# Optimization experiments

Hardware: AMD Instinct MI355X
Metric: run time of the kernel (lower is better)

## Reference

```python
import jax, jax.numpy as jnp
import numpy as np

N, D, H, M = 8192, 64, 4096, 2
EPS = 1e-12  # F.normalize eps


def setup_inputs() -> dict:
    key = jax.random.key(0)
    k0, k1, k2, k3, k4 = jax.random.split(key, 5)
    # spins in {-1, +1}
    x = (2 * jax.random.randint(k0, (N, D), 0, 2) - 1).astype(jnp.float32)
    W1 = jax.random.normal(k1, (D, H), jnp.float32) * 0.05
    b1 = jax.random.normal(k2, (H,), jnp.float32) * 0.05
    W2 = jax.random.normal(k3, (H, M), jnp.float32) * 0.05
    b2 = jax.random.normal(k4, (M,), jnp.float32) * 0.05
    return {"x": x, "W1": W1, "b1": b1, "W2": W2, "b2": b2}


def reference(x, W1, b1, W2, b2):
    # Per step d: mask off sites >= d, run MLP, L2-normalize the 2 amplitudes,
    # select psi_pos/psi_neg by the spin at site d, accumulate product.
    n, d_sites = x.shape
    site_idx = jnp.arange(d_sites)

    def step(wav, d):
        mask = (site_idx < d).astype(x.dtype)          # [D], sites 0..d-1 visible
        h = jnp.tanh((x * mask) @ W1 + b1)             # [N, H]
        out = jnp.tanh(h @ W2 + b2)                    # [N, 2]
        norm = jnp.maximum(
            jnp.sqrt(jnp.sum(out * out, axis=1, keepdims=True)), EPS)
        out = out / norm                               # F.normalize(out, 2)
        sel = jnp.where(x[:, d] > 0, out[:, 0], out[:, 1])
        return wav * sel, None

    wav0 = jnp.ones((n,), x.dtype)
    wav, _ = jax.lax.scan(step, wav0, jnp.arange(d_sites))
    return wav
```

## Files before the change

### kernel.cpp

```cpp
#include <hip/hip_runtime.h>
#include <math.h>

#define NS 8192
#define DS 64
#define HD 4096
#define C2L 2.8853900817779268f
#define CH 4
#define NCH (DS / CH)

typedef float v2f __attribute__((ext_vector_type(2)));

__device__ __forceinline__ v2f pk_add(v2f a, v2f b) {
    v2f d; asm("v_pk_add_f32 %0, %1, %2" : "=v"(d) : "v"(a), "v"(b)); return d;
}
__device__ __forceinline__ v2f pk_mul(v2f a, v2f b) {
    v2f d; asm("v_pk_mul_f32 %0, %1, %2" : "=v"(d) : "v"(a), "v"(b)); return d;
}
__device__ __forceinline__ v2f pk_fma(v2f a, v2f b, v2f c) {
    v2f d; asm("v_pk_fma_f32 %0, %1, %2, %3" : "=v"(d) : "v"(a), "v"(b), "v"(c)); return d;
}

__device__ __forceinline__ float fast_tanh(float x) {
    float t = __builtin_amdgcn_exp2f(x * C2L);
    float r = __builtin_amdgcn_rcpf(t + 1.0f);
    return __builtin_fmaf(-2.0f, r, 1.0f);
}

template <int PATT>
__device__ __forceinline__ v2f swz_xor(v2f v) {
    v2f d;
    d.x = __int_as_float(__builtin_amdgcn_ds_swizzle(__float_as_int(v.x), PATT));
    d.y = __int_as_float(__builtin_amdgcn_ds_swizzle(__float_as_int(v.y), PATT));
    return d;
}

__global__ __launch_bounds__(256) void qnade_prep_E(
    const float* __restrict__ W1, float* __restrict__ Et)
{
    int i = blockIdx.x * 256 + threadIdx.x;
    float w = W1[i] * C2L;
    Et[i]           = __builtin_amdgcn_exp2f(w);
    Et[DS * HD + i] = __builtin_amdgcn_exp2f(-w);
}

__global__ __launch_bounds__(256) void qnade_prep_S(
    const float* __restrict__ W2, const float* __restrict__ b2, float* __restrict__ C01)
{
    __shared__ float p0[4], p1[4];
    int tid = threadIdx.x;
    float s0 = 0.0f, s1 = 0.0f;
    for (int h = tid; h < HD; h += 256) {
        float2 w = ((const float2*)W2)[h];
        s0 += w.x; s1 += w.y;
    }
    #pragma unroll
    for (int m = 1; m < 64; m <<= 1) {
        s0 += __shfl_xor(s0, m, 64);
        s1 += __shfl_xor(s1, m, 64);
    }
    if ((tid & 63) == 0) { p0[tid >> 6] = s0; p1[tid >> 6] = s1; }
    __syncthreads();
    if (tid == 0) {
        C01[0] = p0[0] + p0[1] + p0[2] + p0[3] + b2[0];
        C01[1] = p1[0] + p1[1] + p1[2] + p1[3] + b2[1];
    }
}

#define EV(S, N) e##S##N
#define TV(S, N) t##S##N

#define CHAIN(S, MIDX, SLOT) do {                                             \
    v2f q1 = pk_add(TV(S,0), one);                                            \
    v2f q2 = pk_fma(q1, TV(S,1), q1);                                         \
    v2f q3 = pk_fma(q2, TV(S,2), q2);                                         \
    v2f q4 = pk_fma(q3, TV(S,3), q3);                                         \
    v2f q5 = pk_fma(q4, TV(S,4), q4);                                         \
    v2f q6 = pk_fma(q5, TV(S,5), q5);                                         \
    v2f q7 = pk_fma(q6, TV(S,6), q6);                                         \
    v2f q8 = pk_fma(q7, TV(S,7), q7);                                         \
    float P = q8.x * q8.y;                                                    \
    float R = __builtin_amdgcn_rcpf(P);                                       \
    v2f RR = (v2f){R * q8.y, R * q8.x};                                       \
    v2f r7 = pk_mul(RR, q7);                                                  \
    v2f A0 = pk_mul(r7, w20[7]);                                              \
    v2f A1 = pk_mul(r7, w21[7]);                                              \
    RR = pk_fma(RR, TV(S,7), RR);                                             \
    v2f r6 = pk_mul(RR, q6); A0 = pk_fma(r6, w20[6], A0); A1 = pk_fma(r6, w21[6], A1); RR = pk_fma(RR, TV(S,6), RR); \
    v2f r5 = pk_mul(RR, q5); A0 = pk_fma(r5, w20[5], A0); A1 = pk_fma(r5, w21[5], A1); RR = pk_fma(RR, TV(S,5), RR); \
    v2f r4 = pk_mul(RR, q4); A0 = pk_fma(r4, w20[4], A0); A1 = pk_fma(r4, w21[4], A1); RR = pk_fma(RR, TV(S,4), RR); \
    v2f r3 = pk_mul(RR, q3); A0 = pk_fma(r3, w20[3], A0); A1 = pk_fma(r3, w21[3], A1); RR = pk_fma(RR, TV(S,3), RR); \
    v2f r2 = pk_mul(RR, q2); A0 = pk_fma(r2, w20[2], A0); A1 = pk_fma(r2, w21[2], A1); RR = pk_fma(RR, TV(S,2), RR); \
    v2f r1 = pk_mul(RR, q1); A0 = pk_fma(r1, w20[1], A0); A1 = pk_fma(r1, w21[1], A1); RR = pk_fma(RR, TV(S,1), RR); \
    A0 = pk_fma(RR, w20[0], A0); A1 = pk_fma(RR, w21[0], A1);                 \
    parts[SLOT][MIDX][tid] = make_float2(A0.x + A0.y, A1.x + A1.y);           \
} while (0)

#define TUPD(S) do {                                                          \
    TV(S,0) = pk_mul(TV(S,0), (v2f){EV(S,0).x, EV(S,0).y});                   \
    TV(S,1) = pk_mul(TV(S,1), (v2f){EV(S,0).z, EV(S,0).w});                   \
    TV(S,2) = pk_mul(TV(S,2), (v2f){EV(S,1).x, EV(S,1).y});                   \
    TV(S,3) = pk_mul(TV(S,3), (v2f){EV(S,1).z, EV(S,1).w});                   \
    TV(S,4) = pk_mul(TV(S,4), (v2f){EV(S,2).x, EV(S,2).y});                   \
    TV(S,5) = pk_mul(TV(S,5), (v2f){EV(S,2).z, EV(S,2).w});                   \
    TV(S,6) = pk_mul(TV(S,6), (v2f){EV(S,3).x, EV(S,3).y});                   \
    TV(S,7) = pk_mul(TV(S,7), (v2f){EV(S,3).z, EV(S,3).w});                   \
} while (0)

#define LOADE(S) do {                                                         \
    unsigned off_ = (((msk##S >> nd) & 1ull) ? 0u : (unsigned)(DS * HD)) + nd * (unsigned)HD; \
    const float4* ep_ = (const float4*)(Et + off_) + tq;                      \
    EV(S,0) = ep_[0]; EV(S,1) = ep_[256]; EV(S,2) = ep_[512]; EV(S,3) = ep_[768]; \
} while (0)

__global__ __launch_bounds__(256, 2) void qnade_main(
    const float* __restrict__ x, const float* __restrict__ b1,
    const float* __restrict__ W2, const float* __restrict__ Et,
    const float* __restrict__ C01, float* __restrict__ out)
{
    __shared__ float2 parts[CH][4][256];
    __shared__ float2 fin[4][DS];

    const int tid  = threadIdx.x;
    const int lane = tid & 63;
    const int wv   = tid >> 6;
    const int n0   = blockIdx.x * 4;
    const int eb   = tid * 4;
    const int tq   = tid;

    v2f w20[8], w21[8];
    #pragma unroll
    for (int q = 0; q < 4; ++q) {
        const float4* p = (const float4*)(W2 + 2 * (eb + q * 1024));
        float4 A = p[0], B = p[1];
        w20[2*q]   = (v2f){A.x, A.z};  w21[2*q]   = (v2f){A.y, A.w};
        w20[2*q+1] = (v2f){B.x, B.z};  w21[2*q+1] = (v2f){B.y, B.w};
    }

    v2f i0, i1, i2, i3, i4, i5, i6, i7;
    {
        float4 ba = *(const float4*)(b1 + eb);
        float4 bb = *(const float4*)(b1 + eb + 1024);
        float4 bc = *(const float4*)(b1 + eb + 2048);
        float4 bd = *(const float4*)(b1 + eb + 3072);
        i0 = (v2f){__builtin_amdgcn_exp2f(ba.x * C2L), __builtin_amdgcn_exp2f(ba.y * C2L)};
        i1 = (v2f){__builtin_amdgcn_exp2f(ba.z * C2L), __builtin_amdgcn_exp2f(ba.w * C2L)};
        i2 = (v2f){__builtin_amdgcn_exp2f(bb.x * C2L), __builtin_amdgcn_exp2f(bb.y * C2L)};
        i3 = (v2f){__builtin_amdgcn_exp2f(bb.z * C2L), __builtin_amdgcn_exp2f(bb.w * C2L)};
        i4 = (v2f){__builtin_amdgcn_exp2f(bc.x * C2L), __builtin_amdgcn_exp2f(bc.y * C2L)};
        i5 = (v2f){__builtin_amdgcn_exp2f(bc.z * C2L), __builtin_amdgcn_exp2f(bc.w * C2L)};
        i6 = (v2f){__builtin_amdgcn_exp2f(bd.x * C2L), __builtin_amdgcn_exp2f(bd.y * C2L)};
        i7 = (v2f){__builtin_amdgcn_exp2f(bd.z * C2L), __builtin_amdgcn_exp2f(bd.w * C2L)};
    }
    v2f tA0=i0,tA1=i1,tA2=i2,tA3=i3,tA4=i4,tA5=i5,tA6=i6,tA7=i7;
    v2f tB0=i0,tB1=i1,tB2=i2,tB3=i3,tB4=i4,tB5=i5,tB6=i6,tB7=i7;
    v2f tC0=i0,tC1=i1,tC2=i2,tC3=i3,tC4=i4,tC5=i5,tC6=i6,tC7=i7;
    v2f tD0=i0,tD1=i1,tD2=i2,tD3=i3,tD4=i4,tD5=i5,tD6=i6,tD7=i7;

    const unsigned long long mskA = __ballot(x[(n0 + 0) * DS + lane] > 0.0f);
    const unsigned long long mskB = __ballot(x[(n0 + 1) * DS + lane] > 0.0f);
    const unsigned long long mskC = __ballot(x[(n0 + 2) * DS + lane] > 0.0f);
    const unsigned long long mskD = __ballot(x[(n0 + 3) * DS + lane] > 0.0f);
    const v2f one = (v2f){1.0f, 1.0f};

    float4 eA0, eA1, eA2, eA3, eB0, eB1, eB2, eB3;
    float4 eC0, eC1, eC2, eC3, eD0, eD1, eD2, eD3;

    unsigned nd = 0;
    LOADE(A); LOADE(B); LOADE(C); LOADE(D);

    int d = 0;
    for (int cc = 0; cc < NCH; ++cc) {
        for (int s4 = 0; s4 < CH; ++s4, ++d) {
            CHAIN(A, 0, s4);
            CHAIN(B, 1, s4);
            CHAIN(C, 2, s4);
            CHAIN(D, 3, s4);
            TUPD(A); TUPD(B); TUPD(C); TUPD(D);
            nd = (unsigned)(d + 1) & (DS - 1);
            LOADE(A); LOADE(B); LOADE(C); LOADE(D);
        }

        __syncthreads();
        {
            const int j  = tid & 15;
            const int u  = tid >> 4;
            const int m  = u & 3;
            const int sr = u >> 2;
            v2f s = (v2f){0.0f, 0.0f};
            #pragma unroll
            for (int i = 0; i < 16; ++i) {
                float2 v = parts[sr][m][j + 16 * i];
                s = pk_add(s, (v2f){v.x, v.y});
            }
            s = pk_add(s, swz_xor<0x041F>(s));
            s = pk_add(s, swz_xor<0x081F>(s));
            s = pk_add(s, swz_xor<0x101F>(s));
            s = pk_add(s, swz_xor<0x201F>(s));
            if (j == 0) fin[m][cc * CH + sr] = make_float2(s.x, s.y);
        }
        __syncthreads();
    }

    {
        const unsigned long long mm = (wv == 0) ? mskA : (wv == 1) ? mskB
                                    : (wv == 2) ? mskC : mskD;
        float2 sv = fin[wv][lane];
        float dot0 = __builtin_fmaf(-2.0f, sv.x, C01[0]);
        float dot1 = __builtin_fmaf(-2.0f, sv.y, C01[1]);
        float o0 = fast_tanh(dot0);
        float o1 = fast_tanh(dot1);
        float nrm = sqrtf(__builtin_fmaf(o0, o0, o1 * o1));
        nrm = fmaxf(nrm, 1e-12f);
        float sel = ((mm >> lane) & 1ull) ? o0 : o1;
        float v = sel * __builtin_amdgcn_rcpf(nrm);
        v *= __shfl_xor(v, 1, 64);
        v *= __shfl_xor(v, 2, 64);
        v *= __shfl_xor(v, 4, 64);
        v *= __shfl_xor(v, 8, 64);
        v *= __shfl_xor(v, 16, 64);
        v *= __shfl_xor(v, 32, 64);
        if (lane == 0) out[n0 + wv] = v;
    }
}

__global__ __launch_bounds__(256) void qnade_fallback(
    const float* __restrict__ x, const float* __restrict__ W1,
    const float* __restrict__ b1, const float* __restrict__ W2,
    const float* __restrict__ b2, float* __restrict__ out)
{
    __shared__ __align__(16) float w20s[HD];
    __shared__ __align__(16) float w21s[HD];
    const int tid = threadIdx.x;
    for (int i = tid; i < HD; i += 256) {
        float2 w = ((const float2*)W2)[i];
        w20s[i] = w.x;
        w21s[i] = w.y;
    }
    const int lane = tid & 63;
    const int wv   = tid >> 6;
    const int n    = (blockIdx.x << 2) + wv;
    const float b20 = b2[0];
    const float b21 = b2[1];
    const float xv = x[n * DS + lane];
    float4 a[16];
    const float4* b1v = (const float4*)b1;
    #pragma unroll
    for (int q = 0; q < 16; ++q) a[q] = b1v[q * 64 + lane];
    __syncthreads();
    const float4* w20v = (const float4*)w20s;
    const float4* w21v = (const float4*)w21s;
    float wav = 1.0f;
    for (int d = 0; d < DS; ++d) {
        const float xd = __shfl(xv, d, 64);
        const float4* w1v = (const float4*)(W1 + d * HD);
        float dot0 = 0.0f, dot1 = 0.0f;
        #pragma unroll
        for (int q = 0; q < 16; ++q) {
            float4 w1 = w1v[q * 64 + lane];
            float4 av = a[q];
            float h0 = fast_tanh(av.x);
            float h1 = fast_tanh(av.y);
            float h2 = fast_tanh(av.z);
            float h3 = fast_tanh(av.w);
            float4 c0 = w20v[q * 64 + lane];
            float4 c1 = w21v[q * 64 + lane];
            dot0 = fmaf(h0, c0.x, dot0); dot0 = fmaf(h1, c0.y, dot0);
            dot0 = fmaf(h2, c0.z, dot0); dot0 = fmaf(h3, c0.w, dot0);
            dot1 = fmaf(h0, c1.x, dot1); dot1 = fmaf(h1, c1.y, dot1);
            dot1 = fmaf(h2, c1.z, dot1); dot1 = fmaf(h3, c1.w, dot1);
            av.x = fmaf(xd, w1.x, av.x); av.y = fmaf(xd, w1.y, av.y);
            av.z = fmaf(xd, w1.z, av.z); av.w = fmaf(xd, w1.w, av.w);
            a[q] = av;
        }
        #pragma unroll
        for (int m = 1; m < 64; m <<= 1) {
            dot0 += __shfl_xor(dot0, m, 64);
            dot1 += __shfl_xor(dot1, m, 64);
        }
        float o0 = fast_tanh(dot0 + b20);
        float o1 = fast_tanh(dot1 + b21);
        float nrm = sqrtf(fmaf(o0, o0, o1 * o1));
        nrm = fmaxf(nrm, 1e-12f);
        float sel = (xd > 0.0f) ? o0 : o1;
        wav *= sel / nrm;
    }
    out[n] = wav;
}

extern "C" void kernel_launch(void* const* d_in, const int* in_sizes, int n_in,
                              void* d_out, int out_size, void* d_ws, size_t ws_size,
                              hipStream_t stream) {
    const float* x  = (const float*)d_in[0];
    const float* W1 = (const float*)d_in[1];
    const float* b1 = (const float*)d_in[2];
    const float* W2 = (const float*)d_in[3];
    const float* b2 = (const float*)d_in[4];
    float* out = (float*)d_out;

    const size_t need = (size_t)(2 * DS * HD + 2) * sizeof(float);
    if (ws_size >= need) {
        float* Et  = (float*)d_ws;
        float* C01 = Et + 2 * DS * HD;
        hipLaunchKernelGGL(qnade_prep_E, dim3(DS * HD / 256), dim3(256), 0, stream, W1, Et);
        hipLaunchKernelGGL(qnade_prep_S, dim3(1), dim3(256), 0, stream, W2, b2, C01);
        hipLaunchKernelGGL(qnade_main, dim3(NS / 4), dim3(256), 0, stream, x, b1, W2, Et, C01, out);
    } else {
        hipLaunchKernelGGL(qnade_fallback, dim3(NS / 4), dim3(256), 0, stream, x, W1, b1, W2, b2, out);
    }
}
```

Measured before the change: 426.3 us.

## Process two samples per block with double-buffered E loads and higher occupancy

```diff
diff --git a/kernel.cpp b/kernel.cpp
--- a/kernel.cpp
+++ b/kernel.cpp
@@ -5,7 +5,7 @@
 #define DS 64
 #define HD 4096
 #define C2L 2.8853900817779268f
-#define CH 4
+#define CH 8
 #define NCH (DS / CH)
 
 typedef float v2f __attribute__((ext_vector_type(2)));
@@ -66,8 +66,9 @@
     }
 }
 
+#define TV(S, N) t##S##N
 #define EV(S, N) e##S##N
-#define TV(S, N) t##S##N
+#define FV(S, N) f##S##N
 
 #define CHAIN(S, MIDX, SLOT) do {                                             \
     v2f q1 = pk_add(TV(S,0), one);                                            \
@@ -92,10 +93,10 @@
     v2f r2 = pk_mul(RR, q2); A0 = pk_fma(r2, w20[2], A0); A1 = pk_fma(r2, w21[2], A1); RR = pk_fma(RR, TV(S,2), RR); \
     v2f r1 = pk_mul(RR, q1); A0 = pk_fma(r1, w20[1], A0); A1 = pk_fma(r1, w21[1], A1); RR = pk_fma(RR, TV(S,1), RR); \
     A0 = pk_fma(RR, w20[0], A0); A1 = pk_fma(RR, w21[0], A1);                 \
-    parts[SLOT][MIDX][tid] = make_float2(A0.x + A0.y, A1.x + A1.y);           \
-} while (0)
-
-#define TUPD(S) do {                                                          \
+    parts[MIDX][SLOT][tid] = make_float2(A0.x + A0.y, A1.x + A1.y);           \
+} while (0)
+
+#define TUPD_E(S) do {                                                        \
     TV(S,0) = pk_mul(TV(S,0), (v2f){EV(S,0).x, EV(S,0).y});                   \
     TV(S,1) = pk_mul(TV(S,1), (v2f){EV(S,0).z, EV(S,0).w});                   \
     TV(S,2) = pk_mul(TV(S,2), (v2f){EV(S,1).x, EV(S,1).y});                   \
@@ -106,90 +107,109 @@
     TV(S,7) = pk_mul(TV(S,7), (v2f){EV(S,3).z, EV(S,3).w});                   \
 } while (0)
 
-#define LOADE(S) do {                                                         \
+#define TUPD_F(S) do {                                                        \
+    TV(S,0) = pk_mul(TV(S,0), (v2f){FV(S,0).x, FV(S,0).y});                   \
+    TV(S,1) = pk_mul(TV(S,1), (v2f){FV(S,0).z, FV(S,0).w});                   \
+    TV(S,2) = pk_mul(TV(S,2), (v2f){FV(S,1).x, FV(S,1).y});                   \
+    TV(S,3) = pk_mul(TV(S,3), (v2f){FV(S,1).z, FV(S,1).w});                   \
+    TV(S,4) = pk_mul(TV(S,4), (v2f){FV(S,2).x, FV(S,2).y});                   \
+    TV(S,5) = pk_mul(TV(S,5), (v2f){FV(S,2).z, FV(S,2).w});                   \
+    TV(S,6) = pk_mul(TV(S,6), (v2f){FV(S,3).x, FV(S,3).y});                   \
+    TV(S,7) = pk_mul(TV(S,7), (v2f){FV(S,3).z, FV(S,3).w});                   \
+} while (0)
+
+#define LOAD_E(S) do {                                                        \
     unsigned off_ = (((msk##S >> nd) & 1ull) ? 0u : (unsigned)(DS * HD)) + nd * (unsigned)HD; \
     const float4* ep_ = (const float4*)(Et + off_) + tq;                      \
-    EV(S,0) = ep_[0]; EV(S,1) = ep_[256]; EV(S,2) = ep_[512]; EV(S,3) = ep_[768]; \
-} while (0)
-
-__global__ __launch_bounds__(256, 2) void qnade_main(
+    EV(S,0) = ep_[0]; EV(S,1) = ep_[64]; EV(S,2) = ep_[128]; EV(S,3) = ep_[192]; \
+} while (0)
+
+#define LOAD_F(S) do {                                                        \
+    unsigned off_ = (((msk##S >> nd) & 1ull) ? 0u : (unsigned)(DS * HD)) + nd * (unsigned)HD; \
+    const float4* ep_ = (const float4*)(Et + off_) + tq;                      \
+    FV(S,0) = ep_[0]; FV(S,1) = ep_[64]; FV(S,2) = ep_[128]; FV(S,3) = ep_[192]; \
+} while (0)
+
+__global__ __launch_bounds__(256, 3) void qnade_main(
     const float* __restrict__ x, const float* __restrict__ b1,
     const float* __restrict__ W2, const float* __restrict__ Et,
     const float* __restrict__ C01, float* __restrict__ out)
 {
-    __shared__ float2 parts[CH][4][256];
-    __shared__ float2 fin[4][DS];
+    __shared__ float2 parts[2][CH][256];
+    __shared__ float2 fin[2][DS];
 
     const int tid  = threadIdx.x;
     const int lane = tid & 63;
     const int wv   = tid >> 6;
-    const int n0   = blockIdx.x * 4;
-    const int eb   = tid * 4;
-    const int tq   = tid;
+    const int n0   = blockIdx.x * 2;
+    const int hbase = wv * 1024 + lane * 4;
+    const int tq    = wv * 256 + lane;
 
     v2f w20[8], w21[8];
     #pragma unroll
     for (int q = 0; q < 4; ++q) {
-        const float4* p = (const float4*)(W2 + 2 * (eb + q * 1024));
+        const float4* p = (const float4*)(W2 + 2 * (hbase + q * 256));
         float4 A = p[0], B = p[1];
         w20[2*q]   = (v2f){A.x, A.z};  w21[2*q]   = (v2f){A.y, A.w};
         w20[2*q+1] = (v2f){B.x, B.z};  w21[2*q+1] = (v2f){B.y, B.w};
     }
 
-    v2f i0, i1, i2, i3, i4, i5, i6, i7;
+    v2f tA0, tA1, tA2, tA3, tA4, tA5, tA6, tA7;
     {
-        float4 ba = *(const float4*)(b1 + eb);
-        float4 bb = *(const float4*)(b1 + eb + 1024);
-        float4 bc = *(const float4*)(b1 + eb + 2048);
-        float4 bd = *(const float4*)(b1 + eb + 3072);
-        i0 = (v2f){__builtin_amdgcn_exp2f(ba.x * C2L), __builtin_amdgcn_exp2f(ba.y * C2L)};
-        i1 = (v2f){__builtin_amdgcn_exp2f(ba.z * C2L), __builtin_amdgcn_exp2f(ba.w * C2L)};
-        i2 = (v2f){__builtin_amdgcn_exp2f(bb.x * C2L), __builtin_amdgcn_exp2f(bb.y * C2L)};
-        i3 = (v2f){__builtin_amdgcn_exp2f(bb.z * C2L), __builtin_amdgcn_exp2f(bb.w * C2L)};
-        i4 = (v2f){__builtin_amdgcn_exp2f(bc.x * C2L), __builtin_amdgcn_exp2f(bc.y * C2L)};
-        i5 = (v2f){__builtin_amdgcn_exp2f(bc.z * C2L), __builtin_amdgcn_exp2f(bc.w * C2L)};
-        i6 = (v2f){__builtin_amdgcn_exp2f(bd.x * C2L), __builtin_amdgcn_exp2f(bd.y * C2L)};
-        i7 = (v2f){__builtin_amdgcn_exp2f(bd.z * C2L), __builtin_amdgcn_exp2f(bd.w * C2L)};
-    }
-    v2f tA0=i0,tA1=i1,tA2=i2,tA3=i3,tA4=i4,tA5=i5,tA6=i6,tA7=i7;
-    v2f tB0=i0,tB1=i1,tB2=i2,tB3=i3,tB4=i4,tB5=i5,tB6=i6,tB7=i7;
-    v2f tC0=i0,tC1=i1,tC2=i2,tC3=i3,tC4=i4,tC5=i5,tC6=i6,tC7=i7;
-    v2f tD0=i0,tD1=i1,tD2=i2,tD3=i3,tD4=i4,tD5=i5,tD6=i6,tD7=i7;
-
-    const unsigned long long mskA = __ballot(x[(n0 + 0) * DS + lane] > 0.0f);
+        float4 b0 = *(const float4*)(b1 + hbase);
+        float4 b1q = *(const float4*)(b1 + hbase + 256);
+        float4 b2q = *(const float4*)(b1 + hbase + 512);
+        float4 b3q = *(const float4*)(b1 + hbase + 768);
+        tA0 = (v2f){__builtin_amdgcn_exp2f(b0.x * C2L), __builtin_amdgcn_exp2f(b0.y * C2L)};
+        tA1 = (v2f){__builtin_amdgcn_exp2f(b0.z * C2L), __builtin_amdgcn_exp2f(b0.w * C2L)};
+        tA2 = (v2f){__builtin_amdgcn_exp2f(b1q.x * C2L), __builtin_amdgcn_exp2f(b1q.y * C2L)};
+        tA3 = (v2f){__builtin_amdgcn_exp2f(b1q.z * C2L), __builtin_amdgcn_exp2f(b1q.w * C2L)};
+        tA4 = (v2f){__builtin_amdgcn_exp2f(b2q.x * C2L), __builtin_amdgcn_exp2f(b2q.y * C2L)};
+        tA5 = (v2f){__builtin_amdgcn_exp2f(b2q.z * C2L), __builtin_amdgcn_exp2f(b2q.w * C2L)};
+        tA6 = (v2f){__builtin_amdgcn_exp2f(b3q.x * C2L), __builtin_amdgcn_exp2f(b3q.y * C2L)};
+        tA7 = (v2f){__builtin_amdgcn_exp2f(b3q.z * C2L), __builtin_amdgcn_exp2f(b3q.w * C2L)};
+    }
+    v2f tB0=tA0, tB1=tA1, tB2=tA2, tB3=tA3, tB4=tA4, tB5=tA5, tB6=tA6, tB7=tA7;
+
+    const unsigned long long mskA = __ballot(x[n0 * DS + lane] > 0.0f);
     const unsigned long long mskB = __ballot(x[(n0 + 1) * DS + lane] > 0.0f);
-    const unsigned long long mskC = __ballot(x[(n0 + 2) * DS + lane] > 0.0f);
-    const unsigned long long mskD = __ballot(x[(n0 + 3) * DS + lane] > 0.0f);
     const v2f one = (v2f){1.0f, 1.0f};
 
     float4 eA0, eA1, eA2, eA3, eB0, eB1, eB2, eB3;
-    float4 eC0, eC1, eC2, eC3, eD0, eD1, eD2, eD3;
+    float4 fA0, fA1, fA2, fA3, fB0, fB1, fB2, fB3;
 
     unsigned nd = 0;
-    LOADE(A); LOADE(B); LOADE(C); LOADE(D);
+    LOAD_E(A); LOAD_E(B);
+    nd = 1;
+    LOAD_F(A); LOAD_F(B);
 
     int d = 0;
     for (int cc = 0; cc < NCH; ++cc) {
-        for (int s4 = 0; s4 < CH; ++s4, ++d) {
-            CHAIN(A, 0, s4);
-            CHAIN(B, 1, s4);
-            CHAIN(C, 2, s4);
-            CHAIN(D, 3, s4);
-            TUPD(A); TUPD(B); TUPD(C); TUPD(D);
-            nd = (unsigned)(d + 1) & (DS - 1);
-            LOADE(A); LOADE(B); LOADE(C); LOADE(D);
+        for (int s8 = 0; s8 < CH; s8 += 2) {
+            CHAIN(A, 0, s8);
+            CHAIN(B, 1, s8);
+            TUPD_E(A); TUPD_E(B);
+            nd = (unsigned)(d + 2) & (DS - 1);
+            LOAD_E(A); LOAD_E(B);
+            ++d;
+            CHAIN(A, 0, s8 + 1);
+            CHAIN(B, 1, s8 + 1);
+            TUPD_F(A); TUPD_F(B);
+            nd = (unsigned)(d + 2) & (DS - 1);
+            LOAD_F(A); LOAD_F(B);
+            ++d;
         }
 
         __syncthreads();
         {
             const int j  = tid & 15;
             const int u  = tid >> 4;
-            const int m  = u & 3;
-            const int sr = u >> 2;
+            const int m  = u & 1;
+            const int sr = u >> 1;
             v2f s = (v2f){0.0f, 0.0f};
             #pragma unroll
             for (int i = 0; i < 16; ++i) {
-                float2 v = parts[sr][m][j + 16 * i];
+                float2 v = parts[m][sr][j + 16 * i];
                 s = pk_add(s, (v2f){v.x, v.y});
             }
             s = pk_add(s, swz_xor<0x041F>(s));
@@ -201,9 +221,8 @@
         __syncthreads();
     }
 
-    {
-        const unsigned long long mm = (wv == 0) ? mskA : (wv == 1) ? mskB
-                                    : (wv == 2) ? mskC : mskD;
+    if (wv < 2) {
+        const unsigned long long mm = wv ? mskB : mskA;
         float2 sv = fin[wv][lane];
         float dot0 = __builtin_fmaf(-2.0f, sv.x, C01[0]);
         float dot1 = __builtin_fmaf(-2.0f, sv.y, C01[1]);
@@ -303,7 +322,7 @@
         float* C01 = Et + 2 * DS * HD;
         hipLaunchKernelGGL(qnade_prep_E, dim3(DS * HD / 256), dim3(256), 0, stream, W1, Et);
         hipLaunchKernelGGL(qnade_prep_S, dim3(1), dim3(256), 0, stream, W2, b2, C01);
-        hipLaunchKernelGGL(qnade_main, dim3(NS / 4), dim3(256), 0, stream, x, b1, W2, Et, C01, out);
+        hipLaunchKernelGGL(qnade_main, dim3(NS / 2), dim3(256), 0, stream, x, b1, W2, Et, C01, out);
     } else {
         hipLaunchKernelGGL(qnade_fallback, dim3(NS / 4), dim3(256), 0, stream, x, W1, b1, W2, b2, out);
     }
```

Measured after the change: 410.9 us. -3.6%, faster.
